# Kernel tuning notes

Hardware: AMD Instinct MI355X
Metric: run time of the kernel (lower is better)

## Reference

```python
import jax, jax.numpy as jnp
import numpy as np

HID = 128

def _gru_states(x, w_ih, w_hh, b_ih, b_hh):
    # x: [B,T,I]; w_ih: [3H,I]; w_hh: [3H,H]; biases: [3H]
    # Precompute input projections for all timesteps (one big GEMM).
    gi = jnp.einsum('bti,gi->tbg', x, w_ih) + b_ih  # [T,B,3H]
    B = x.shape[0]
    h0 = jnp.zeros((B, HID), dtype=x.dtype)

    def step(h, gi_t):
        gh = h @ w_hh.T + b_hh                      # [B,3H]
        i_r, i_z, i_n = jnp.split(gi_t, 3, axis=-1)
        h_r, h_z, h_n = jnp.split(gh, 3, axis=-1)
        r = jax.nn.sigmoid(i_r + h_r)
        z = jax.nn.sigmoid(i_z + h_z)
        n = jnp.tanh(i_n + r * h_n)
        h_new = (1.0 - z) * n + z * h
        return h_new, h_new

    _, states = jax.lax.scan(step, h0, gi)          # states: [T,B,H]
    return states


def setup_inputs() -> dict:
    key = jax.random.key(0)
    ks = jax.random.split(key, 7)
    B, T, I, H, E = 64, 2048, 128, HID, 64
    s_ih = 1.0 / np.sqrt(I)
    s_hh = 1.0 / np.sqrt(H)
    s_p = 1.0 / np.sqrt(H)
    return {
        'x': jax.random.normal(ks[0], (B, T, I), dtype=jnp.float32),
        'w_ih': jax.random.uniform(ks[1], (3 * H, I), jnp.float32, -s_ih, s_ih),
        'w_hh': jax.random.uniform(ks[2], (3 * H, H), jnp.float32, -s_hh, s_hh),
        'b_ih': jax.random.uniform(ks[3], (3 * H,), jnp.float32, -s_hh, s_hh),
        'b_hh': jax.random.uniform(ks[4], (3 * H,), jnp.float32, -s_hh, s_hh),
        'w_proj': jax.random.uniform(ks[5], (E, H), jnp.float32, -s_p, s_p),
        'b_proj': jax.random.uniform(ks[6], (E,), jnp.float32, -s_p, s_p),
    }


def reference(x, w_ih, w_hh, b_ih, b_hh, w_proj, b_proj):
    states = _gru_states(x, w_ih, w_hh, b_ih, b_hh)  # [T,B,H]
    pooled = states.mean(axis=0)                     # mean pooling over time -> [B,H]
    return pooled @ w_proj.T + b_proj                # [B,E]
```

## Files before the change

### kernel.cpp

```cpp
#include <hip/hip_runtime.h>
#include <math.h>

#define B_   64
#define T_   2048
#define HID_ 128
#define G3_  384
#define IN_  128
#define E_   64

#define TS_  128

typedef _Float16 h2f  __attribute__((ext_vector_type(2)));
typedef _Float16 f16x8 __attribute__((ext_vector_type(8)));
typedef float    f32x4 __attribute__((ext_vector_type(4)));

__device__ __forceinline__ float rcp_(float x)     { return __builtin_amdgcn_rcpf(x); }
__device__ __forceinline__ float sigmoid_(float x) { return rcp_(1.f + __expf(-x)); }
__device__ __forceinline__ float tanh_(float x)    { return 1.f - 2.f * rcp_(1.f + __expf(2.f * x)); }

__device__ __forceinline__ f16x8 pack8_(float4 a, float4 b) {
    uint4 u;
    u.x = __builtin_bit_cast(unsigned, __builtin_amdgcn_cvt_pkrtz(a.x, a.y));
    u.y = __builtin_bit_cast(unsigned, __builtin_amdgcn_cvt_pkrtz(a.z, a.w));
    u.z = __builtin_bit_cast(unsigned, __builtin_amdgcn_cvt_pkrtz(b.x, b.y));
    u.w = __builtin_bit_cast(unsigned, __builtin_amdgcn_cvt_pkrtz(b.z, b.w));
    return __builtin_bit_cast(f16x8, u);
}

__global__ __launch_bounds__(256, 1)
void gi_gemm(const float* __restrict__ x, const float* __restrict__ w_ih,
             const float* __restrict__ b_ih, const float* __restrict__ b_hh,
             float* __restrict__ gi, int t0)
{
    const int tid = threadIdx.x;
    const int w   = tid >> 6;
    const int l   = tid & 63;
    const int ln  = l & 15;
    const int kq  = l >> 4;
    const int tt  = blockIdx.x;
    const int b   = blockIdx.y;
    const int tl_base = tt * TS_ + w * 32;

    float bias_r[24];
    #pragma unroll
    for (int nt = 0; nt < 24; nt++) {
        const int col = nt * 16 + ln;
        bias_r[nt] = b_ih[col] + (col < 256 ? b_hh[col] : 0.f);
    }

    f32x4 acc[2][24];
    #pragma unroll
    for (int mt = 0; mt < 2; mt++)
        #pragma unroll
        for (int nt = 0; nt < 24; nt++)
            acc[mt][nt] = (f32x4){0.f, 0.f, 0.f, 0.f};

    const float* xb = x + ((size_t)b * T_ + (size_t)(t0 + tl_base)) * IN_;

    #pragma unroll
    for (int kc = 0; kc < 4; kc++) {
        const int ko = kc * 32 + kq * 8;
        f16x8 afr[2];
        #pragma unroll
        for (int mt = 0; mt < 2; mt++) {
            const float* xr = xb + (size_t)(mt * 16 + ln) * IN_ + ko;
            float4 p0 = *reinterpret_cast<const float4*>(xr);
            float4 p1 = *reinterpret_cast<const float4*>(xr + 4);
            afr[mt] = pack8_(p0, p1);
        }
        #pragma unroll
        for (int nt = 0; nt < 24; nt++) {
            const float* wr = w_ih + (size_t)(nt * 16 + ln) * IN_ + ko;
            float4 q0 = *reinterpret_cast<const float4*>(wr);
            float4 q1 = *reinterpret_cast<const float4*>(wr + 4);
            const f16x8 bfr = pack8_(q0, q1);
            acc[0][nt] = __builtin_amdgcn_mfma_f32_16x16x32_f16(afr[0], bfr, acc[0][nt], 0, 0, 0);
            acc[1][nt] = __builtin_amdgcn_mfma_f32_16x16x32_f16(afr[1], bfr, acc[1][nt], 0, 0, 0);
        }
    }

    #pragma unroll
    for (int mt = 0; mt < 2; mt++) {
        #pragma unroll
        for (int r = 0; r < 4; r++) {
            const size_t trow = (size_t)(tl_base + mt * 16 + kq * 4 + r);
            float* go = gi + trow * (B_ * G3_) + (size_t)b * G3_ + ln;
            #pragma unroll
            for (int nt = 0; nt < 24; nt++)
                go[nt * 16] = acc[mt][nt][r] + bias_r[nt];
        }
    }
}

#define REC_STEP(CUR, LD, TLOAD, PB)                                           \
  {                                                                            \
    const float* gp_ = gib + (size_t)(TLOAD) * S;                              \
    LD[0] = gp_[c0];       LD[1] = gp_[c0 + 64];                               \
    LD[2] = gp_[c0 + 128]; LD[3] = gp_[c0 + 192];                              \
    LD[4] = gp_[c0 + 256]; LD[5] = gp_[c0 + 320];                              \
    const char* hb_ = (const char*)(&h2_sh[PB][0]) + kq * 16;                  \
    f16x8 af_[4];                                                              \
    af_[0] = __builtin_bit_cast(f16x8, *(const uint4*)(hb_));                  \
    af_[1] = __builtin_bit_cast(f16x8, *(const uint4*)(hb_ + 64));             \
    af_[2] = __builtin_bit_cast(f16x8, *(const uint4*)(hb_ + 128));            \
    af_[3] = __builtin_bit_cast(f16x8, *(const uint4*)(hb_ + 192));            \
    f32x4 ac_[6];                                                              \
    _Pragma("unroll")                                                          \
    for (int m = 0; m < 6; m++) ac_[m] = (f32x4){0.f, 0.f, 0.f, 0.f};          \
    _Pragma("unroll")                                                          \
    for (int kc = 0; kc < 4; kc++) {                                           \
      _Pragma("unroll")                                                        \
      for (int m = 0; m < 6; m++)                                              \
        ac_[m] = __builtin_amdgcn_mfma_f32_16x16x32_f16(af_[kc], wfr[m][kc],   \
                                                        ac_[m], 0, 0, 0);      \
    }                                                                          \
    const float r0 = sigmoid_(CUR[0] + ac_[0][0]);                             \
    const float r1 = sigmoid_(CUR[1] + ac_[1][0]);                             \
    const float z0 = sigmoid_(CUR[2] + ac_[2][0]);                             \
    const float z1 = sigmoid_(CUR[3] + ac_[3][0]);                             \
    const float n0 = tanh_(CUR[4] + r0 * (ac_[4][0] + bh0));                   \
    const float n1 = tanh_(CUR[5] + r1 * (ac_[5][0] + bh1));                   \
    hj0 = (1.f - z0) * n0 + z0 * hj0;                                          \
    hj1 = (1.f - z1) * n1 + z1 * hj1;                                          \
    hs0 += hj0; hs1 += hj1;                                                    \
    if (kq == 0) {                                                             \
      h2_sh[(PB) ^ 1][c0] = (_Float16)hj0;                                     \
      h2_sh[(PB) ^ 1][c1] = (_Float16)hj1;                                     \
    }                                                                          \
    __syncthreads();                                                           \
  }

__global__ __launch_bounds__(256, 1)
void rec_kernel(const float* __restrict__ gi, const float* __restrict__ w_hh,
                const float* __restrict__ b_hh,
                const float* __restrict__ w_proj, const float* __restrict__ b_proj,
                float* __restrict__ out, float* __restrict__ state,
                int t0, int t1)
{
    const int tid  = threadIdx.x;
    const int b    = blockIdx.x;
    const int w    = tid >> 6;
    const int lane = tid & 63;
    const int ln   = lane & 15;
    const int kq   = lane >> 4;
    const int c0   = 16 * w + ln;
    const int c1   = c0 + 64;
    const int nT   = t1 - t0;

    __shared__ _Float16 h2_sh[2][HID_];
    __shared__ float pooled[HID_];

    f16x8 wfr[6][4];
    #pragma unroll
    for (int m = 0; m < 6; m++) {
        const float* wr = w_hh + (size_t)(c0 + 64 * m) * HID_;
        #pragma unroll
        for (int kc = 0; kc < 4; kc++) {
            const float* p = wr + kc * 32 + kq * 8;
            float4 q0 = *reinterpret_cast<const float4*>(p);
            float4 q1 = *reinterpret_cast<const float4*>(p + 4);
            wfr[m][kc] = pack8_(q0, q1);
        }
    }
    const float bh0 = b_hh[256 + c0];
    const float bh1 = b_hh[256 + c1];

    float hj0, hj1, hs0, hs1;
    if (t0 == 0) { hj0 = hj1 = hs0 = hs1 = 0.f; }
    else {
        hj0 = state[b * HID_ + c0];             hj1 = state[b * HID_ + c1];
        hs0 = state[B_ * HID_ + b * HID_ + c0]; hs1 = state[B_ * HID_ + b * HID_ + c1];
    }
    if (kq == 0) {
        h2_sh[0][c0] = (_Float16)hj0;
        h2_sh[0][c1] = (_Float16)hj1;
    }
    __syncthreads();

    const float* gib = gi + (size_t)b * G3_;
    const size_t S = (size_t)B_ * G3_;

    float g0[6], g1[6], g2[6], g3[6];
    {
        const float* p0 = gib;
        const float* p1 = gib + S;
        g0[0]=p0[c0]; g0[1]=p0[c0+64]; g0[2]=p0[c0+128]; g0[3]=p0[c0+192]; g0[4]=p0[c0+256]; g0[5]=p0[c0+320];
        g1[0]=p1[c0]; g1[1]=p1[c0+64]; g1[2]=p1[c0+128]; g1[3]=p1[c0+192]; g1[4]=p1[c0+256]; g1[5]=p1[c0+320];
    }

    int pb = 0;
    for (int t = 0; t < nT; t += 4) {
        const int nTm1 = nT - 1;
        int t2 = t + 2 < nTm1 ? t + 2 : nTm1;
        int t3 = t + 3 < nTm1 ? t + 3 : nTm1;
        int t4 = t + 4 < nTm1 ? t + 4 : nTm1;
        int t5 = t + 5 < nTm1 ? t + 5 : nTm1;
        REC_STEP(g0, g2, t2, pb); pb ^= 1;
        REC_STEP(g1, g3, t3, pb); pb ^= 1;
        REC_STEP(g2, g0, t4, pb); pb ^= 1;
        REC_STEP(g3, g1, t5, pb); pb ^= 1;
    }

    if (t1 < T_) {
        if (kq == 0) {
            state[b * HID_ + c0]             = hj0;  state[b * HID_ + c1]             = hj1;
            state[B_ * HID_ + b * HID_ + c0] = hs0;  state[B_ * HID_ + b * HID_ + c1] = hs1;
        }
    } else {
        if (kq == 0) {
            pooled[c0] = hs0 * (1.f / (float)T_);
            pooled[c1] = hs1 * (1.f / (float)T_);
        }
        __syncthreads();
        if (tid < E_) {
            const float4* wpj = reinterpret_cast<const float4*>(w_proj + (size_t)tid * HID_);
            const float4* pp  = reinterpret_cast<const float4*>(pooled);
            float a0 = 0.f, a1 = 0.f, a2 = 0.f, a3 = 0.f;
            #pragma unroll
            for (int k = 0; k < 32; k++) {
                float4 wv = wpj[k]; float4 pv = pp[k];
                a0 = fmaf(wv.x, pv.x, a0);
                a1 = fmaf(wv.y, pv.y, a1);
                a2 = fmaf(wv.z, pv.z, a2);
                a3 = fmaf(wv.w, pv.w, a3);
            }
            out[b * E_ + tid] = (a0 + a1) + (a2 + a3) + b_proj[tid];
        }
    }
}

extern "C" void kernel_launch(void* const* d_in, const int* in_sizes, int n_in,
                              void* d_out, int out_size, void* d_ws, size_t ws_size,
                              hipStream_t stream)
{
    const float* x      = (const float*)d_in[0];
    const float* w_ih   = (const float*)d_in[1];
    const float* w_hh   = (const float*)d_in[2];
    const float* b_ih   = (const float*)d_in[3];
    const float* b_hh   = (const float*)d_in[4];
    const float* w_proj = (const float*)d_in[5];
    const float* b_proj = (const float*)d_in[6];
    float* out = (float*)d_out;

    const size_t state_bytes = (size_t)2 * B_ * HID_ * sizeof(float);
    const size_t per_t = (size_t)B_ * G3_ * sizeof(float);
    size_t avail = ws_size > state_bytes ? ws_size - state_bytes : 0;
    int chunkT = (int)(avail / per_t);
    if (chunkT > T_) chunkT = T_;
    chunkT &= ~(TS_ - 1);
    if (chunkT < TS_) chunkT = TS_;

    float* gi_buf = (float*)d_ws;
    float* state  = (float*)((char*)d_ws + (size_t)chunkT * per_t);

    for (int t0 = 0; t0 < T_; t0 += chunkT) {
        int t1 = t0 + chunkT; if (t1 > T_) t1 = T_;
        int nT = t1 - t0;
        gi_gemm<<<dim3(nT / TS_, B_), dim3(256), 0, stream>>>(x, w_ih, b_ih, b_hh, gi_buf, t0);
        rec_kernel<<<dim3(B_), dim3(256), 0, stream>>>(gi_buf, w_hh, b_hh, w_proj, b_proj,
                                                       out, state, t0, t1);
    }
}
```

Before: 987.0 us.

## Repartition gi GEMM warps over output columns and keep W_ih fragments in registers

Each of the four warps now owns a 96-column slice of the gate output across all 128 timesteps of the tile, instead of a 32-row slice across all 384 columns. Its W_ih fragments (6 column tiles by 4 k-chunks) are loaded and converted to fp16 once and kept in registers. This removes the repeated per-warp loading and packing of the whole weight matrix. In exchange, every warp reads and converts all 128 x rows, so x global traffic per block grows fourfold. Register pressure stays comparable, with 48 accumulators plus 24 weight fragments against 48 accumulators before.

```diff
diff --git a/kernel.cpp b/kernel.cpp
--- a/kernel.cpp
+++ b/kernel.cpp
@@ -39,55 +39,60 @@
     const int kq  = l >> 4;
     const int tt  = blockIdx.x;
     const int b   = blockIdx.y;
-    const int tl_base = tt * TS_ + w * 32;
-
-    float bias_r[24];
-    #pragma unroll
-    for (int nt = 0; nt < 24; nt++) {
-        const int col = nt * 16 + ln;
-        bias_r[nt] = b_ih[col] + (col < 256 ? b_hh[col] : 0.f);
-    }
-
-    f32x4 acc[2][24];
-    #pragma unroll
-    for (int mt = 0; mt < 2; mt++)
-        #pragma unroll
-        for (int nt = 0; nt < 24; nt++)
-            acc[mt][nt] = (f32x4){0.f, 0.f, 0.f, 0.f};
-
-    const float* xb = x + ((size_t)b * T_ + (size_t)(t0 + tl_base)) * IN_;
+
+    f16x8 wfr[6][4];
+    float bias[6];
+    #pragma unroll
+    for (int i = 0; i < 6; i++) {
+        const int col = (6 * w + i) * 16 + ln;
+        const float* wr = w_ih + (size_t)col * IN_;
+        #pragma unroll
+        for (int kc = 0; kc < 4; kc++) {
+            const float* p = wr + kc * 32 + kq * 8;
+            float4 q0 = *reinterpret_cast<const float4*>(p);
+            float4 q1 = *reinterpret_cast<const float4*>(p + 4);
+            wfr[i][kc] = pack8_(q0, q1);
+        }
+        bias[i] = b_ih[col] + (col < 256 ? b_hh[col] : 0.f);
+    }
+
+    f32x4 acc[8][6];
+    #pragma unroll
+    for (int mt = 0; mt < 8; mt++)
+        #pragma unroll
+        for (int i = 0; i < 6; i++)
+            acc[mt][i] = (f32x4){0.f, 0.f, 0.f, 0.f};
+
+    const float* xb = x + ((size_t)b * T_ + (size_t)(t0 + tt * TS_)) * IN_;
 
     #pragma unroll
     for (int kc = 0; kc < 4; kc++) {
         const int ko = kc * 32 + kq * 8;
-        f16x8 afr[2];
-        #pragma unroll
-        for (int mt = 0; mt < 2; mt++) {
+        f16x8 afr[8];
+        #pragma unroll
+        for (int mt = 0; mt < 8; mt++) {
             const float* xr = xb + (size_t)(mt * 16 + ln) * IN_ + ko;
             float4 p0 = *reinterpret_cast<const float4*>(xr);
             float4 p1 = *reinterpret_cast<const float4*>(xr + 4);
             afr[mt] = pack8_(p0, p1);
         }
         #pragma unroll
-        for (int nt = 0; nt < 24; nt++) {
-            const float* wr = w_ih + (size_t)(nt * 16 + ln) * IN_ + ko;
-            float4 q0 = *reinterpret_cast<const float4*>(wr);
-            float4 q1 = *reinterpret_cast<const float4*>(wr + 4);
-            const f16x8 bfr = pack8_(q0, q1);
-            acc[0][nt] = __builtin_amdgcn_mfma_f32_16x16x32_f16(afr[0], bfr, acc[0][nt], 0, 0, 0);
-            acc[1][nt] = __builtin_amdgcn_mfma_f32_16x16x32_f16(afr[1], bfr, acc[1][nt], 0, 0, 0);
-        }
-    }
-
-    #pragma unroll
-    for (int mt = 0; mt < 2; mt++) {
+        for (int i = 0; i < 6; i++)
+            #pragma unroll
+            for (int mt = 0; mt < 8; mt++)
+                acc[mt][i] = __builtin_amdgcn_mfma_f32_16x16x32_f16(afr[mt], wfr[i][kc],
+                                                                   acc[mt][i], 0, 0, 0);
+    }
+
+    #pragma unroll
+    for (int mt = 0; mt < 8; mt++) {
         #pragma unroll
         for (int r = 0; r < 4; r++) {
-            const size_t trow = (size_t)(tl_base + mt * 16 + kq * 4 + r);
-            float* go = gi + trow * (B_ * G3_) + (size_t)b * G3_ + ln;
+            const size_t trow = (size_t)(tt * TS_ + mt * 16 + kq * 4 + r);
+            float* go = gi + trow * (B_ * G3_) + (size_t)b * G3_ + (size_t)(6 * w) * 16 + ln;
             #pragma unroll
-            for (int nt = 0; nt < 24; nt++)
-                go[nt * 16] = acc[mt][nt][r] + bias_r[nt];
+            for (int i = 0; i < 6; i++)
+                go[i * 16] = acc[mt][i][r] + bias[i];
         }
     }
 }
```

After: 1.007 ms. +2.1%, slower.
